# Performance work log

Hardware: AMD Instinct MI355X
Metric: run time of the kernel (lower is better)

The kernel has to match this reference:

```python
import jax, jax.numpy as jnp
import numpy as np

N_NODES = 100000


def gcn_conv(x, W, b, src, dst, n_nodes):
    # PyG GCNConv: x' = x @ W; symmetric deg^-1/2 normalization with self-loops; scatter-add; + bias
    h = x @ W  # [N, out]
    ones = jnp.ones(dst.shape[0], dtype=h.dtype)
    deg = jax.ops.segment_sum(ones, dst, num_segments=n_nodes)  # in-degree incl. self-loops
    dinv = jnp.where(deg > 0, jax.lax.rsqrt(deg), 0.0)
    norm = dinv[src] * dinv[dst]                      # [E]
    msgs = h[src] * norm[:, None]                     # gather + scale, [E, out]
    out = jax.ops.segment_sum(msgs, dst, num_segments=n_nodes)  # scatter-add
    return out + b


def setup_inputs() -> dict:
    key = jax.random.key(0)
    ks = jax.random.split(key, 8)
    n, e, din, dh, dout = N_NODES, 1600000, 32, 64, 5
    x = jax.random.normal(ks[0], (n, din), dtype=jnp.float32)
    edge_index = jax.random.randint(ks[1], (2, e), 0, n, dtype=jnp.int64)
    W1 = jax.random.normal(ks[2], (din, dh), dtype=jnp.float32) * (1.0 / np.sqrt(din))
    b1 = jax.random.normal(ks[3], (dh,), dtype=jnp.float32) * 0.02
    W2 = jax.random.normal(ks[4], (dh, dh), dtype=jnp.float32) * (1.0 / np.sqrt(dh))
    b2 = jax.random.normal(ks[5], (dh,), dtype=jnp.float32) * 0.02
    Wfc = jax.random.normal(ks[6], (dh, dout), dtype=jnp.float32) * (1.0 / np.sqrt(dh))
    bfc = jax.random.normal(ks[7], (dout,), dtype=jnp.float32) * 0.02
    return {"x": x, "edge_index": edge_index, "W1": W1, "b1": b1,
            "W2": W2, "b2": b2, "Wfc": Wfc, "bfc": bfc}


def reference(x, edge_index, W1, b1, W2, b2, Wfc, bfc):
    n = x.shape[0]
    loops = jnp.arange(n, dtype=edge_index.dtype)
    src = jnp.concatenate([edge_index[0], loops])  # add self-loops (PyG default)
    dst = jnp.concatenate([edge_index[1], loops])
    h = jax.nn.relu(gcn_conv(x, W1, b1, src, dst, n))
    h = jax.nn.relu(gcn_conv(h, W2, b2, src, dst, n))
    g = jnp.mean(h, axis=0)          # mean pool over nodes, [hidden]
    logits = g @ Wfc + bfc           # [output_dim]
    return jax.nn.log_softmax(logits, axis=0)
```

## Files before the change

kernel.cpp:

```cpp
#include <hip/hip_runtime.h>
#include <math.h>

#define NBLK 256

typedef unsigned int uint;
typedef __attribute__((ext_vector_type(8))) short short8;
typedef __attribute__((ext_vector_type(4))) float f32x4;
typedef __attribute__((ext_vector_type(2))) float f32x2;

#if defined(__has_builtin)
#if __has_builtin(__builtin_amdgcn_cvt_pk_f32_fp8) && __has_builtin(__builtin_amdgcn_cvt_pk_fp8_f32)
#define HW_FP8 1
#endif
#endif
#ifndef HW_FP8
#define HW_FP8 0
#endif

__device__ __forceinline__ uint pack_bf16(float a, float b) {
    uint ua = __float_as_uint(a), ub = __float_as_uint(b);
    ua = (ua + 0x7fffu + ((ua >> 16) & 1u)) >> 16;
    ub = (ub + 0x7fffu + ((ub >> 16) & 1u)) >> 16;
    return ua | (ub << 16);
}

__device__ __forceinline__ uint fp8_enc_sw(float v) {
    uint u = __float_as_uint(v);
    uint s = (u >> 24) & 0x80u;
    uint a = u & 0x7fffffffu;
    if (a < 0x3BF80000u) return s;
    if (a >= 0x43F80000u) return s | 0x7Fu;
    uint r = a + 0x0007FFFFu + ((a >> 20) & 1u);
    uint e8 = (r >> 23) - 120u;
    return s | (e8 << 3) | ((r >> 20) & 7u);
}
__device__ __forceinline__ float fp8_dec_sw(uint b) {
    uint t = b & 0x7fu;
    uint h = ((b & 0x80u) << 8) | (t ? ((t << 7) + 0x2000u) : 0u);
    return (float)__builtin_bit_cast(_Float16, (unsigned short)h);
}

__device__ __forceinline__ uint fp8x2_enc(float a, float b) {
#if HW_FP8
    return (uint)__builtin_amdgcn_cvt_pk_fp8_f32(a, b, 0, false);
#else
    return fp8_enc_sw(a) | (fp8_enc_sw(b) << 8);
#endif
}


__global__ void pass_hist(const int* __restrict__ dst, int* __restrict__ cnt,
                          int E, int nbucket, int chunk) {
    extern __shared__ int h[];
    int blk = blockIdx.x;
    for (int i = threadIdx.x; i < nbucket; i += blockDim.x) h[i] = 0;
    __syncthreads();
    int lo = blk * chunk, hi = min(lo + chunk, E);
    for (int e = lo + threadIdx.x; e < hi; e += blockDim.x)
        atomicAdd(&h[dst[e] >> 8], 1);
    __syncthreads();
    for (int i = threadIdx.x; i < nbucket; i += blockDim.x)
        cnt[i * NBLK + blk] = h[i];
}

__global__ void row_scan(int* __restrict__ cnt, int* __restrict__ totals) {
    __shared__ int lds[NBLK];
    int b = blockIdx.x, t = threadIdx.x;
    int v = cnt[b * NBLK + t];
    lds[t] = v;
    __syncthreads();
    for (int off = 1; off < NBLK; off <<= 1) {
        int y = (t >= off) ? lds[t - off] : 0;
        __syncthreads();
        lds[t] += y;
        __syncthreads();
    }
    cnt[b * NBLK + t] = lds[t] - v;
    if (t == NBLK - 1) totals[b] = lds[NBLK - 1];
}

__global__ void total_scan(int* __restrict__ totals, int nb) {
    __shared__ int lds[256];
    __shared__ int carry;
    int t = threadIdx.x;
    if (t == 0) carry = 0;
    __syncthreads();
    for (int c = 0; c < nb; c += 256) {
        int v = (c + t < nb) ? totals[c + t] : 0;
        lds[t] = v;
        __syncthreads();
        for (int off = 1; off < 256; off <<= 1) {
            int y = (t >= off) ? lds[t - off] : 0;
            __syncthreads();
            lds[t] += y;
            __syncthreads();
        }
        if (c + t < nb) totals[c + t] = carry + lds[t] - v;
        __syncthreads();
        if (t == 0) carry += lds[255];
        __syncthreads();
    }
    if (t == 0) totals[nb] = carry;
}

__global__ void pass_scatter(const int* __restrict__ src, const int* __restrict__ dst,
                             const int* __restrict__ cnt, const int* __restrict__ totals,
                             int* __restrict__ bucketed, int E, int nbucket, int chunk) {
    extern __shared__ int lcur[];
    int blk = blockIdx.x;
    for (int i = threadIdx.x; i < nbucket; i += blockDim.x)
        lcur[i] = cnt[i * NBLK + blk] + totals[i];
    __syncthreads();
    int lo = blk * chunk, hi = min(lo + chunk, E);
    for (int e = lo + threadIdx.x; e < hi; e += blockDim.x) {
        int s = src[e], d = dst[e];
        int pos = atomicAdd(&lcur[d >> 8], 1);
        bucketed[pos] = (s << 8) | (d & 255);
    }
}

__global__ void bucket_finalize(const int* __restrict__ bucketed, const int* __restrict__ totals,
                                int* __restrict__ rowptr, float* __restrict__ dinv,
                                int* __restrict__ csr_src, int n) {
    __shared__ int deg[256], sc[256], lcur[256];
    int b = blockIdx.x, t = threadIdx.x;
    int base = totals[b], bend = totals[b + 1];
    deg[t] = 0;
    __syncthreads();
    for (int i = base + t; i < bend; i += 256)
        atomicAdd(&deg[bucketed[i] & 255], 1);
    __syncthreads();
    int v = deg[t];
    sc[t] = v;
    __syncthreads();
    for (int off = 1; off < 256; off <<= 1) {
        int y = (t >= off) ? sc[t - off] : 0;
        __syncthreads();
        sc[t] += y;
        __syncthreads();
    }
    int ex = sc[t] - v;
    lcur[t] = ex;
    int node = b * 256 + t;
    if (node < n) {
        rowptr[node] = base + ex;
        dinv[node] = rsqrtf((float)(v + 1));
    }
    if (b == 0 && t == 0) rowptr[n] = totals[gridDim.x];
    __syncthreads();
    for (int i = base + t; i < bend; i += 256) {
        int p = bucketed[i];
        int pos = atomicAdd(&lcur[p & 255], 1);
        csr_src[base + pos] = p >> 8;
    }
}


__global__ void convert_x_fp8(const float* __restrict__ x, const float* __restrict__ dinv,
                              uint* __restrict__ xfp8, int n) {
    int i = blockIdx.x * blockDim.x + threadIdx.x;
    if (i >= n * 8) return;
    int v = i >> 3;
    float di = dinv[v];
    float4 xr = reinterpret_cast<const float4*>(x)[i];
    uint lo = fp8x2_enc(xr.x * di, xr.y * di);
    uint hi = fp8x2_enc(xr.z * di, xr.w * di);
    xfp8[i] = (lo & 0xffffu) | (hi << 16);
}


#if HW_FP8
#define DEC8ACC(U)                                                         \
    do {                                                                   \
        f32x2 p0 = __builtin_amdgcn_cvt_pk_f32_fp8((int)(U).x, 0);         \
        f32x2 p1 = __builtin_amdgcn_cvt_pk_f32_fp8((int)(U).x, 1);         \
        f32x2 p2 = __builtin_amdgcn_cvt_pk_f32_fp8((int)(U).y, 0);         \
        f32x2 p3 = __builtin_amdgcn_cvt_pk_f32_fp8((int)(U).y, 1);         \
        a0 += p0.x; a1 += p0.y; a2 += p1.x; a3 += p1.y;                    \
        a4 += p2.x; a5 += p2.y; a6 += p3.x; a7 += p3.y;                    \
    } while (0)
#else
#define DEC8ACC(U)                                                         \
    do {                                                                   \
        a0 += fp8_dec_sw((U).x); a1 += fp8_dec_sw((U).x >> 8);             \
        a2 += fp8_dec_sw((U).x >> 16); a3 += fp8_dec_sw((U).x >> 24);      \
        a4 += fp8_dec_sw((U).y); a5 += fp8_dec_sw((U).y >> 8);             \
        a6 += fp8_dec_sw((U).y >> 16); a7 += fp8_dec_sw((U).y >> 24);      \
    } while (0)
#endif

template <int LOG_NSL>
__global__ __launch_bounds__(256, 4) void agg_gather_fp8(
    const int* __restrict__ rowptr, const int* __restrict__ csr_src,
    const float* __restrict__ dinv, const uint* __restrict__ feat,
    uint* __restrict__ out, int n, int npad) {
    int bid = blockIdx.x;
    int slice = bid & ((1 << LOG_NSL) - 1);
    int chunk = bid >> LOG_NSL;
    int node = chunk * 64 + (threadIdx.x >> 2);
    if (node >= n) return;
    int q = threadIdx.x & 3;
    const uint* fs = feat + (size_t)slice * npad * 8 + q * 2;
    int k = rowptr[node], end = rowptr[node + 1];
    float a0 = 0.f, a1 = 0.f, a2 = 0.f, a3 = 0.f, a4 = 0.f, a5 = 0.f, a6 = 0.f, a7 = 0.f;
    {
        uint2 w = *reinterpret_cast<const uint2*>(fs + (size_t)node * 8);
        DEC8ACC(w);
    }
    for (; k + 4 <= end; k += 4) {
        int s0 = csr_src[k], s1 = csr_src[k + 1], s2 = csr_src[k + 2], s3 = csr_src[k + 3];
        uint2 u0 = *reinterpret_cast<const uint2*>(fs + (size_t)s0 * 8);
        uint2 u1 = *reinterpret_cast<const uint2*>(fs + (size_t)s1 * 8);
        uint2 u2 = *reinterpret_cast<const uint2*>(fs + (size_t)s2 * 8);
        uint2 u3 = *reinterpret_cast<const uint2*>(fs + (size_t)s3 * 8);
        DEC8ACC(u0); DEC8ACC(u1); DEC8ACC(u2); DEC8ACC(u3);
    }
    for (; k < end; ++k) {
        int s = csr_src[k];
        uint2 u = *reinterpret_cast<const uint2*>(fs + (size_t)s * 8);
        DEC8ACC(u);
    }
    float di = dinv[node];
    uint4 o;
    o.x = pack_bf16(a0 * di, a1 * di);
    o.y = pack_bf16(a2 * di, a3 * di);
    o.z = pack_bf16(a4 * di, a5 * di);
    o.w = pack_bf16(a6 * di, a7 * di);
    *reinterpret_cast<uint4*>(
        out + ((size_t)((slice << 1) + (q >> 1)) * npad + node) * 8 + (q & 1) * 4) = o;
}


__device__ __forceinline__ short8 make_bfrag(const float* __restrict__ W, int kbase, int col) {
    uint w0 = pack_bf16(W[(kbase + 0) * 64 + col], W[(kbase + 1) * 64 + col]);
    uint w1 = pack_bf16(W[(kbase + 2) * 64 + col], W[(kbase + 3) * 64 + col]);
    uint w2 = pack_bf16(W[(kbase + 4) * 64 + col], W[(kbase + 5) * 64 + col]);
    uint w3 = pack_bf16(W[(kbase + 6) * 64 + col], W[(kbase + 7) * 64 + col]);
    uint4 u; u.x = w0; u.y = w1; u.z = w2; u.w = w3;
    return __builtin_bit_cast(short8, u);
}

__global__ __launch_bounds__(256) void gemm1_mfma(const uint* __restrict__ A,
                                                  const float* __restrict__ W,
                                                  const float* __restrict__ bias,
                                                  const float* __restrict__ dinv,
                                                  uint* __restrict__ outw, int n, int npad) {
    int t = threadIdx.x;
    int lane = t & 63, wv = t >> 6;
    int rowbase = blockIdx.x * 64 + wv * 16;
    int r16 = lane & 15, g4 = lane >> 4;
    short8 a = __builtin_bit_cast(short8, *reinterpret_cast<const uint4*>(
        A + ((size_t)(g4 >> 1) * npad + rowbase + r16) * 8 + (g4 & 1) * 4));
    int kbase = g4 * 8;
    float dr[4];
#pragma unroll
    for (int r = 0; r < 4; ++r) {
        int row = rowbase + g4 * 4 + r;
        dr[r] = (row < n) ? dinv[row] : 0.f;
    }
#pragma unroll
    for (int nt = 0; nt < 4; ++nt) {
        int col = nt * 16 + r16;
        short8 b = make_bfrag(W, kbase, col);
        f32x4 z = {0.f, 0.f, 0.f, 0.f};
        f32x4 acc = __builtin_amdgcn_mfma_f32_16x16x32_bf16(a, b, z, 0, 0, 0);
        float bcol = bias[col];
#pragma unroll
        for (int r = 0; r < 4; ++r) {
            int row = rowbase + g4 * 4 + r;
            float v = fmaxf(acc[r] + bcol, 0.f) * dr[r];
            float vn = __shfl_xor(v, 1);
            uint e = fp8x2_enc(v, vn) & 0xffffu;
            uint e2 = __shfl_xor(e, 2);
            if ((r16 & 3) == 0)
                outw[((size_t)(col >> 5) * npad + row) * 8 + ((col & 31) >> 2)] =
                    e | (e2 << 16);
        }
    }
}

__global__ __launch_bounds__(256) void gemm2_mfma_pool(const uint* __restrict__ A,
                                                       const float* __restrict__ W,
                                                       const float* __restrict__ bias,
                                                       float* __restrict__ pool_part,
                                                       int n, int npad) {
    __shared__ float sblk[64];
    int t = threadIdx.x;
    if (t < 64) sblk[t] = 0.f;
    __syncthreads();
    int lane = t & 63, wv = t >> 6;
    int rowbase = blockIdx.x * 64 + wv * 16;
    int r16 = lane & 15, g4 = lane >> 4;
    size_t roff = (size_t)(rowbase + r16) * 8 + (g4 & 1) * 4;
    size_t sstride = (size_t)npad * 8;
    short8 a0 = __builtin_bit_cast(short8,
        *reinterpret_cast<const uint4*>(A + (size_t)(g4 >> 1) * sstride + roff));
    short8 a1 = __builtin_bit_cast(short8,
        *reinterpret_cast<const uint4*>(A + (size_t)(2 + (g4 >> 1)) * sstride + roff));
#pragma unroll
    for (int nt = 0; nt < 4; ++nt) {
        int col = nt * 16 + r16;
        short8 b0 = make_bfrag(W, g4 * 8, col);
        short8 b1 = make_bfrag(W, 32 + g4 * 8, col);
        f32x4 z = {0.f, 0.f, 0.f, 0.f};
        f32x4 acc = __builtin_amdgcn_mfma_f32_16x16x32_bf16(a0, b0, z, 0, 0, 0);
        acc = __builtin_amdgcn_mfma_f32_16x16x32_bf16(a1, b1, acc, 0, 0, 0);
        float bcol = bias[col];
        float part = 0.f;
#pragma unroll
        for (int r = 0; r < 4; ++r) {
            int row = rowbase + g4 * 4 + r;
            float v = fmaxf(acc[r] + bcol, 0.f);
            part += (row < n) ? v : 0.f;
        }
        atomicAdd(&sblk[col], part);
    }
    __syncthreads();
    if (t < 64) pool_part[(size_t)blockIdx.x * 64 + t] = sblk[t];
}

__global__ __launch_bounds__(256) void pool_reduce(const float* __restrict__ pool_part,
                                                   int nblk, float* __restrict__ part2) {
    __shared__ float sd[256];
    int t = threadIdx.x;
    int col = t & 63, grp = t >> 6;
    int row0 = blockIdx.x * 4 + grp;
    float acc = 0.f;
    for (int b = row0; b < nblk; b += 256) acc += pool_part[(size_t)b * 64 + col];
    sd[t] = acc;
    __syncthreads();
    if (t < 64)
        part2[(size_t)blockIdx.x * 64 + t] = sd[t] + sd[t + 64] + sd[t + 128] + sd[t + 192];
}

__global__ __launch_bounds__(512) void final_head(const float* __restrict__ part2,
                                                  const float* __restrict__ Wfc,
                                                  const float* __restrict__ bfc,
                                                  float* __restrict__ out, int n) {
    __shared__ float red[512];
    __shared__ float gsh[64];
    __shared__ float logits[5];
    int t = threadIdx.x;
    int col = t & 63, grp = t >> 6;
    float acc = 0.f;
#pragma unroll
    for (int i = 0; i < 8; ++i) acc += part2[(size_t)(grp * 8 + i) * 64 + col];
    red[t] = acc;
    __syncthreads();
    if (t < 64) {
        float s = 0.f;
#pragma unroll
        for (int gI = 0; gI < 8; ++gI) s += red[gI * 64 + t];
        gsh[t] = s;
    }
    __syncthreads();
    if (t < 5) {
        float a = bfc[t];
        float invn = 1.0f / (float)n;
        for (int k = 0; k < 64; ++k) a += (gsh[k] * invn) * Wfc[k * 5 + t];
        logits[t] = a;
    }
    __syncthreads();
    if (t == 0) {
        float m = logits[0];
        for (int i = 1; i < 5; ++i) m = fmaxf(m, logits[i]);
        float s = 0.0f;
        for (int i = 0; i < 5; ++i) s += expf(logits[i] - m);
        float lse = m + logf(s);
        for (int i = 0; i < 5; ++i) out[i] = logits[i] - lse;
    }
}


extern "C" void kernel_launch(void* const* d_in, const int* in_sizes, int n_in,
                              void* d_out, int out_size, void* d_ws, size_t ws_size,
                              hipStream_t stream) {
    const float* x   = (const float*)d_in[0];
    const int*   ei  = (const int*)d_in[1];
    const float* W1  = (const float*)d_in[2];
    const float* b1  = (const float*)d_in[3];
    const float* W2  = (const float*)d_in[4];
    const float* b2  = (const float*)d_in[5];
    const float* Wfc = (const float*)d_in[6];
    const float* bfc = (const float*)d_in[7];
    float* out = (float*)d_out;

    const int n = in_sizes[0] / 32;
    const int E = in_sizes[1] / 2;
    const int* src = ei;
    const int* dst = ei + E;
    const int npad = (n + 63) & ~63;
    const int nbucket = (n + 255) >> 8;
    const int chunk = (E + NBLK - 1) / NBLK;
    const int nchunk = (n + 63) / 64;

    int*   csr_src = (int*)d_ws;
    int*   rowptr  = csr_src + E;
    float* dinv    = (float*)(rowptr + n + 1);
    int*   cnt     = (int*)(dinv + n);
    int*   totals  = cnt + (size_t)nbucket * NBLK;
    size_t offw    = (size_t)(totals + nbucket + 1 - (int*)d_ws);
    offw           = (offw + 3) & ~(size_t)3;
    uint*  xfp8    = (uint*)d_ws + offw;
    uint*  h1fp8   = xfp8 + (size_t)npad * 8;
    uint*  agg1    = h1fp8 + (size_t)2 * npad * 8;
    uint*  agg2    = agg1 + (size_t)2 * npad * 8;
    float* pool_part = (float*)(agg2 + (size_t)4 * npad * 8);
    float* part2   = pool_part + (size_t)nchunk * 64;
    int*   bucketed = (int*)agg2;

    const int B = 256;
    const size_t lds_b = (size_t)nbucket * sizeof(int);

    pass_hist<<<NBLK, B, lds_b, stream>>>(dst, cnt, E, nbucket, chunk);
    row_scan<<<nbucket, NBLK, 0, stream>>>(cnt, totals);
    total_scan<<<1, B, 0, stream>>>(totals, nbucket);
    pass_scatter<<<NBLK, B, lds_b, stream>>>(src, dst, cnt, totals, bucketed, E, nbucket, chunk);
    bucket_finalize<<<nbucket, B, 0, stream>>>(bucketed, totals, rowptr, dinv, csr_src, n);

    convert_x_fp8<<<(n * 8 + B - 1) / B, B, 0, stream>>>(x, dinv, xfp8, n);

    agg_gather_fp8<0><<<nchunk, B, 0, stream>>>(rowptr, csr_src, dinv, xfp8, agg1, n, npad);
    gemm1_mfma<<<nchunk, B, 0, stream>>>(agg1, W1, b1, dinv, h1fp8, n, npad);

    agg_gather_fp8<1><<<nchunk * 2, B, 0, stream>>>(rowptr, csr_src, dinv, h1fp8, agg2, n, npad);
    gemm2_mfma_pool<<<nchunk, B, 0, stream>>>(agg2, W2, b2, pool_part, n, npad);

    pool_reduce<<<64, B, 0, stream>>>(pool_part, nchunk, part2);
    final_head<<<1, 512, 0, stream>>>(part2, Wfc, bfc, out, n);
}
```

Measured before the change: 127.1 us.

## Fuse x fp8 conversion into bucket_finalize and layer-1 gather into GEMM1

The x-to-fp8 conversion (pre-scaled by dinv) now happens inside bucket_finalize, with each node thread converting its own row, so one launch is gone. The layer-1 neighbour gather is fused with the GEMM1 MFMA kernel: aggregated rows are packed to bf16 in LDS and fed straight into the MFMA, removing the agg1 global buffer round trip and another launch. In exchange, the per-thread x conversion in bucket_finalize reads 128 contiguous bytes per thread, which coalesces poorly, and the fused kernel's LDS use may affect occupancy.

```diff
diff --git a/kernel.cpp b/kernel.cpp
--- a/kernel.cpp
+++ b/kernel.cpp
@@ -47,127 +47,6 @@
     return fp8_enc_sw(a) | (fp8_enc_sw(b) << 8);
 #endif
 }
-
-
-__global__ void pass_hist(const int* __restrict__ dst, int* __restrict__ cnt,
-                          int E, int nbucket, int chunk) {
-    extern __shared__ int h[];
-    int blk = blockIdx.x;
-    for (int i = threadIdx.x; i < nbucket; i += blockDim.x) h[i] = 0;
-    __syncthreads();
-    int lo = blk * chunk, hi = min(lo + chunk, E);
-    for (int e = lo + threadIdx.x; e < hi; e += blockDim.x)
-        atomicAdd(&h[dst[e] >> 8], 1);
-    __syncthreads();
-    for (int i = threadIdx.x; i < nbucket; i += blockDim.x)
-        cnt[i * NBLK + blk] = h[i];
-}
-
-__global__ void row_scan(int* __restrict__ cnt, int* __restrict__ totals) {
-    __shared__ int lds[NBLK];
-    int b = blockIdx.x, t = threadIdx.x;
-    int v = cnt[b * NBLK + t];
-    lds[t] = v;
-    __syncthreads();
-    for (int off = 1; off < NBLK; off <<= 1) {
-        int y = (t >= off) ? lds[t - off] : 0;
-        __syncthreads();
-        lds[t] += y;
-        __syncthreads();
-    }
-    cnt[b * NBLK + t] = lds[t] - v;
-    if (t == NBLK - 1) totals[b] = lds[NBLK - 1];
-}
-
-__global__ void total_scan(int* __restrict__ totals, int nb) {
-    __shared__ int lds[256];
-    __shared__ int carry;
-    int t = threadIdx.x;
-    if (t == 0) carry = 0;
-    __syncthreads();
-    for (int c = 0; c < nb; c += 256) {
-        int v = (c + t < nb) ? totals[c + t] : 0;
-        lds[t] = v;
-        __syncthreads();
-        for (int off = 1; off < 256; off <<= 1) {
-            int y = (t >= off) ? lds[t - off] : 0;
-            __syncthreads();
-            lds[t] += y;
-            __syncthreads();
-        }
-        if (c + t < nb) totals[c + t] = carry + lds[t] - v;
-        __syncthreads();
-        if (t == 0) carry += lds[255];
-        __syncthreads();
-    }
-    if (t == 0) totals[nb] = carry;
-}
-
-__global__ void pass_scatter(const int* __restrict__ src, const int* __restrict__ dst,
-                             const int* __restrict__ cnt, const int* __restrict__ totals,
-                             int* __restrict__ bucketed, int E, int nbucket, int chunk) {
-    extern __shared__ int lcur[];
-    int blk = blockIdx.x;
-    for (int i = threadIdx.x; i < nbucket; i += blockDim.x)
-        lcur[i] = cnt[i * NBLK + blk] + totals[i];
-    __syncthreads();
-    int lo = blk * chunk, hi = min(lo + chunk, E);
-    for (int e = lo + threadIdx.x; e < hi; e += blockDim.x) {
-        int s = src[e], d = dst[e];
-        int pos = atomicAdd(&lcur[d >> 8], 1);
-        bucketed[pos] = (s << 8) | (d & 255);
-    }
-}
-
-__global__ void bucket_finalize(const int* __restrict__ bucketed, const int* __restrict__ totals,
-                                int* __restrict__ rowptr, float* __restrict__ dinv,
-                                int* __restrict__ csr_src, int n) {
-    __shared__ int deg[256], sc[256], lcur[256];
-    int b = blockIdx.x, t = threadIdx.x;
-    int base = totals[b], bend = totals[b + 1];
-    deg[t] = 0;
-    __syncthreads();
-    for (int i = base + t; i < bend; i += 256)
-        atomicAdd(&deg[bucketed[i] & 255], 1);
-    __syncthreads();
-    int v = deg[t];
-    sc[t] = v;
-    __syncthreads();
-    for (int off = 1; off < 256; off <<= 1) {
-        int y = (t >= off) ? sc[t - off] : 0;
-        __syncthreads();
-        sc[t] += y;
-        __syncthreads();
-    }
-    int ex = sc[t] - v;
-    lcur[t] = ex;
-    int node = b * 256 + t;
-    if (node < n) {
-        rowptr[node] = base + ex;
-        dinv[node] = rsqrtf((float)(v + 1));
-    }
-    if (b == 0 && t == 0) rowptr[n] = totals[gridDim.x];
-    __syncthreads();
-    for (int i = base + t; i < bend; i += 256) {
-        int p = bucketed[i];
-        int pos = atomicAdd(&lcur[p & 255], 1);
-        csr_src[base + pos] = p >> 8;
-    }
-}
-
-
-__global__ void convert_x_fp8(const float* __restrict__ x, const float* __restrict__ dinv,
-                              uint* __restrict__ xfp8, int n) {
-    int i = blockIdx.x * blockDim.x + threadIdx.x;
-    if (i >= n * 8) return;
-    int v = i >> 3;
-    float di = dinv[v];
-    float4 xr = reinterpret_cast<const float4*>(x)[i];
-    uint lo = fp8x2_enc(xr.x * di, xr.y * di);
-    uint hi = fp8x2_enc(xr.z * di, xr.w * di);
-    xfp8[i] = (lo & 0xffffu) | (hi << 16);
-}
-
 
 #if HW_FP8
 #define DEC8ACC(U)                                                         \
@@ -189,6 +68,209 @@
     } while (0)
 #endif
 
+
+__global__ void pass_hist(const int* __restrict__ dst, int* __restrict__ cnt,
+                          int E, int nbucket, int chunk) {
+    extern __shared__ int h[];
+    int blk = blockIdx.x;
+    for (int i = threadIdx.x; i < nbucket; i += blockDim.x) h[i] = 0;
+    __syncthreads();
+    int lo = blk * chunk, hi = min(lo + chunk, E);
+    for (int e = lo + threadIdx.x; e < hi; e += blockDim.x)
+        atomicAdd(&h[dst[e] >> 8], 1);
+    __syncthreads();
+    for (int i = threadIdx.x; i < nbucket; i += blockDim.x)
+        cnt[i * NBLK + blk] = h[i];
+}
+
+__global__ void row_scan(int* __restrict__ cnt, int* __restrict__ totals) {
+    __shared__ int lds[NBLK];
+    int b = blockIdx.x, t = threadIdx.x;
+    int v = cnt[b * NBLK + t];
+    lds[t] = v;
+    __syncthreads();
+    for (int off = 1; off < NBLK; off <<= 1) {
+        int y = (t >= off) ? lds[t - off] : 0;
+        __syncthreads();
+        lds[t] += y;
+        __syncthreads();
+    }
+    cnt[b * NBLK + t] = lds[t] - v;
+    if (t == NBLK - 1) totals[b] = lds[NBLK - 1];
+}
+
+__global__ void total_scan(int* __restrict__ totals, int nb) {
+    __shared__ int lds[256];
+    __shared__ int carry;
+    int t = threadIdx.x;
+    if (t == 0) carry = 0;
+    __syncthreads();
+    for (int c = 0; c < nb; c += 256) {
+        int v = (c + t < nb) ? totals[c + t] : 0;
+        lds[t] = v;
+        __syncthreads();
+        for (int off = 1; off < 256; off <<= 1) {
+            int y = (t >= off) ? lds[t - off] : 0;
+            __syncthreads();
+            lds[t] += y;
+            __syncthreads();
+        }
+        if (c + t < nb) totals[c + t] = carry + lds[t] - v;
+        __syncthreads();
+        if (t == 0) carry += lds[255];
+        __syncthreads();
+    }
+    if (t == 0) totals[nb] = carry;
+}
+
+__global__ void pass_scatter(const int* __restrict__ src, const int* __restrict__ dst,
+                             const int* __restrict__ cnt, const int* __restrict__ totals,
+                             int* __restrict__ bucketed, int E, int nbucket, int chunk) {
+    extern __shared__ int lcur[];
+    int blk = blockIdx.x;
+    for (int i = threadIdx.x; i < nbucket; i += blockDim.x)
+        lcur[i] = cnt[i * NBLK + blk] + totals[i];
+    __syncthreads();
+    int lo = blk * chunk, hi = min(lo + chunk, E);
+    for (int e = lo + threadIdx.x; e < hi; e += blockDim.x) {
+        int s = src[e], d = dst[e];
+        int pos = atomicAdd(&lcur[d >> 8], 1);
+        bucketed[pos] = (s << 8) | (d & 255);
+    }
+}
+
+__global__ void bucket_finalize(const int* __restrict__ bucketed, const int* __restrict__ totals,
+                                int* __restrict__ rowptr, float* __restrict__ dinv,
+                                int* __restrict__ csr_src, const float* __restrict__ x,
+                                uint* __restrict__ xfp8, int n) {
+    __shared__ int deg[256], sc[256], lcur[256];
+    int b = blockIdx.x, t = threadIdx.x;
+    int base = totals[b], bend = totals[b + 1];
+    deg[t] = 0;
+    __syncthreads();
+    for (int i = base + t; i < bend; i += 256)
+        atomicAdd(&deg[bucketed[i] & 255], 1);
+    __syncthreads();
+    int v = deg[t];
+    sc[t] = v;
+    __syncthreads();
+    for (int off = 1; off < 256; off <<= 1) {
+        int y = (t >= off) ? sc[t - off] : 0;
+        __syncthreads();
+        sc[t] += y;
+        __syncthreads();
+    }
+    int ex = sc[t] - v;
+    lcur[t] = ex;
+    int node = b * 256 + t;
+    if (node < n) {
+        float dfac = rsqrtf((float)(v + 1));
+        rowptr[node] = base + ex;
+        dinv[node] = dfac;
+        const float4* xr = reinterpret_cast<const float4*>(x + (size_t)node * 32);
+        uint* xo = xfp8 + (size_t)node * 8;
+#pragma unroll
+        for (int w = 0; w < 8; ++w) {
+            float4 xv = xr[w];
+            uint lo = fp8x2_enc(xv.x * dfac, xv.y * dfac);
+            uint hi = fp8x2_enc(xv.z * dfac, xv.w * dfac);
+            xo[w] = (lo & 0xffffu) | (hi << 16);
+        }
+    }
+    if (b == 0 && t == 0) rowptr[n] = totals[gridDim.x];
+    __syncthreads();
+    for (int i = base + t; i < bend; i += 256) {
+        int p = bucketed[i];
+        int pos = atomicAdd(&lcur[p & 255], 1);
+        csr_src[base + pos] = p >> 8;
+    }
+}
+
+
+__device__ __forceinline__ short8 make_bfrag(const float* __restrict__ W, int kbase, int col) {
+    uint w0 = pack_bf16(W[(kbase + 0) * 64 + col], W[(kbase + 1) * 64 + col]);
+    uint w1 = pack_bf16(W[(kbase + 2) * 64 + col], W[(kbase + 3) * 64 + col]);
+    uint w2 = pack_bf16(W[(kbase + 4) * 64 + col], W[(kbase + 5) * 64 + col]);
+    uint w3 = pack_bf16(W[(kbase + 6) * 64 + col], W[(kbase + 7) * 64 + col]);
+    uint4 u; u.x = w0; u.y = w1; u.z = w2; u.w = w3;
+    return __builtin_bit_cast(short8, u);
+}
+
+__global__ __launch_bounds__(256, 4) void agg1_gemm1_fused(
+    const int* __restrict__ rowptr, const int* __restrict__ csr_src,
+    const float* __restrict__ dinv, const uint* __restrict__ xfp8,
+    const float* __restrict__ W, const float* __restrict__ bias,
+    uint* __restrict__ outw, int n, int npad) {
+    __shared__ uint lds[64 * 16];
+    int t = threadIdx.x;
+    {
+        int v4 = t >> 2, q = t & 3;
+        int node = blockIdx.x * 64 + v4;
+        const uint* fs = xfp8 + q * 2;
+        float a0 = 0.f, a1 = 0.f, a2 = 0.f, a3 = 0.f,
+              a4 = 0.f, a5 = 0.f, a6 = 0.f, a7 = 0.f;
+        float di = 0.f;
+        int k = 0, end = 0;
+        if (node < n) {
+            k = rowptr[node]; end = rowptr[node + 1];
+            di = dinv[node];
+            uint2 w = *reinterpret_cast<const uint2*>(fs + (size_t)node * 8);
+            DEC8ACC(w);
+        }
+        for (; k + 4 <= end; k += 4) {
+            int s0 = csr_src[k], s1 = csr_src[k + 1], s2 = csr_src[k + 2], s3 = csr_src[k + 3];
+            uint2 u0 = *reinterpret_cast<const uint2*>(fs + (size_t)s0 * 8);
+            uint2 u1 = *reinterpret_cast<const uint2*>(fs + (size_t)s1 * 8);
+            uint2 u2 = *reinterpret_cast<const uint2*>(fs + (size_t)s2 * 8);
+            uint2 u3 = *reinterpret_cast<const uint2*>(fs + (size_t)s3 * 8);
+            DEC8ACC(u0); DEC8ACC(u1); DEC8ACC(u2); DEC8ACC(u3);
+        }
+        for (; k < end; ++k) {
+            int s = csr_src[k];
+            uint2 u = *reinterpret_cast<const uint2*>(fs + (size_t)s * 8);
+            DEC8ACC(u);
+        }
+        uint4 o;
+        o.x = pack_bf16(a0 * di, a1 * di);
+        o.y = pack_bf16(a2 * di, a3 * di);
+        o.z = pack_bf16(a4 * di, a5 * di);
+        o.w = pack_bf16(a6 * di, a7 * di);
+        *reinterpret_cast<uint4*>(&lds[v4 * 16 + q * 4]) = o;
+    }
+    __syncthreads();
+    int lane = t & 63, wv = t >> 6;
+    int rowbase = blockIdx.x * 64 + wv * 16;
+    int r16 = lane & 15, g4 = lane >> 4;
+    short8 a = __builtin_bit_cast(short8,
+        *reinterpret_cast<const uint4*>(&lds[(wv * 16 + r16) * 16 + g4 * 4]));
+    int kbase = g4 * 8;
+    float dr[4];
+#pragma unroll
+    for (int r = 0; r < 4; ++r) {
+        int row = rowbase + g4 * 4 + r;
+        dr[r] = (row < n) ? dinv[row] : 0.f;
+    }
+#pragma unroll
+    for (int nt = 0; nt < 4; ++nt) {
+        int col = nt * 16 + r16;
+        short8 b = make_bfrag(W, kbase, col);
+        f32x4 z = {0.f, 0.f, 0.f, 0.f};
+        f32x4 acc = __builtin_amdgcn_mfma_f32_16x16x32_bf16(a, b, z, 0, 0, 0);
+        float bcol = bias[col];
+#pragma unroll
+        for (int r = 0; r < 4; ++r) {
+            int row = rowbase + g4 * 4 + r;
+            float v = fmaxf(acc[r] + bcol, 0.f) * dr[r];
+            float vn = __shfl_xor(v, 1);
+            uint e = fp8x2_enc(v, vn) & 0xffffu;
+            uint e2 = __shfl_xor(e, 2);
+            if ((r16 & 3) == 0)
+                outw[((size_t)(col >> 5) * npad + row) * 8 + ((col & 31) >> 2)] =
+                    e | (e2 << 16);
+        }
+    }
+}
+
 template <int LOG_NSL>
 __global__ __launch_bounds__(256, 4) void agg_gather_fp8(
     const int* __restrict__ rowptr, const int* __restrict__ csr_src,
@@ -230,55 +312,6 @@
         out + ((size_t)((slice << 1) + (q >> 1)) * npad + node) * 8 + (q & 1) * 4) = o;
 }
 
-
-__device__ __forceinline__ short8 make_bfrag(const float* __restrict__ W, int kbase, int col) {
-    uint w0 = pack_bf16(W[(kbase + 0) * 64 + col], W[(kbase + 1) * 64 + col]);
-    uint w1 = pack_bf16(W[(kbase + 2) * 64 + col], W[(kbase + 3) * 64 + col]);
-    uint w2 = pack_bf16(W[(kbase + 4) * 64 + col], W[(kbase + 5) * 64 + col]);
-    uint w3 = pack_bf16(W[(kbase + 6) * 64 + col], W[(kbase + 7) * 64 + col]);
-    uint4 u; u.x = w0; u.y = w1; u.z = w2; u.w = w3;
-    return __builtin_bit_cast(short8, u);
-}
-
-__global__ __launch_bounds__(256) void gemm1_mfma(const uint* __restrict__ A,
-                                                  const float* __restrict__ W,
-                                                  const float* __restrict__ bias,
-                                                  const float* __restrict__ dinv,
-                                                  uint* __restrict__ outw, int n, int npad) {
-    int t = threadIdx.x;
-    int lane = t & 63, wv = t >> 6;
-    int rowbase = blockIdx.x * 64 + wv * 16;
-    int r16 = lane & 15, g4 = lane >> 4;
-    short8 a = __builtin_bit_cast(short8, *reinterpret_cast<const uint4*>(
-        A + ((size_t)(g4 >> 1) * npad + rowbase + r16) * 8 + (g4 & 1) * 4));
-    int kbase = g4 * 8;
-    float dr[4];
-#pragma unroll
-    for (int r = 0; r < 4; ++r) {
-        int row = rowbase + g4 * 4 + r;
-        dr[r] = (row < n) ? dinv[row] : 0.f;
-    }
-#pragma unroll
-    for (int nt = 0; nt < 4; ++nt) {
-        int col = nt * 16 + r16;
-        short8 b = make_bfrag(W, kbase, col);
-        f32x4 z = {0.f, 0.f, 0.f, 0.f};
-        f32x4 acc = __builtin_amdgcn_mfma_f32_16x16x32_bf16(a, b, z, 0, 0, 0);
-        float bcol = bias[col];
-#pragma unroll
-        for (int r = 0; r < 4; ++r) {
-            int row = rowbase + g4 * 4 + r;
-            float v = fmaxf(acc[r] + bcol, 0.f) * dr[r];
-            float vn = __shfl_xor(v, 1);
-            uint e = fp8x2_enc(v, vn) & 0xffffu;
-            uint e2 = __shfl_xor(e, 2);
-            if ((r16 & 3) == 0)
-                outw[((size_t)(col >> 5) * npad + row) * 8 + ((col & 31) >> 2)] =
-                    e | (e2 << 16);
-        }
-    }
-}
-
 __global__ __launch_bounds__(256) void gemm2_mfma_pool(const uint* __restrict__ A,
                                                        const float* __restrict__ W,
                                                        const float* __restrict__ bias,
@@ -403,8 +436,7 @@
     offw           = (offw + 3) & ~(size_t)3;
     uint*  xfp8    = (uint*)d_ws + offw;
     uint*  h1fp8   = xfp8 + (size_t)npad * 8;
-    uint*  agg1    = h1fp8 + (size_t)2 * npad * 8;
-    uint*  agg2    = agg1 + (size_t)2 * npad * 8;
+    uint*  agg2    = h1fp8 + (size_t)2 * npad * 8;
     float* pool_part = (float*)(agg2 + (size_t)4 * npad * 8);
     float* part2   = pool_part + (size_t)nchunk * 64;
     int*   bucketed = (int*)agg2;
@@ -416,12 +448,11 @@
     row_scan<<<nbucket, NBLK, 0, stream>>>(cnt, totals);
     total_scan<<<1, B, 0, stream>>>(totals, nbucket);
     pass_scatter<<<NBLK, B, lds_b, stream>>>(src, dst, cnt, totals, bucketed, E, nbucket, chunk);
-    bucket_finalize<<<nbucket, B, 0, stream>>>(bucketed, totals, rowptr, dinv, csr_src, n);
-
-    convert_x_fp8<<<(n * 8 + B - 1) / B, B, 0, stream>>>(x, dinv, xfp8, n);
-
-    agg_gather_fp8<0><<<nchunk, B, 0, stream>>>(rowptr, csr_src, dinv, xfp8, agg1, n, npad);
-    gemm1_mfma<<<nchunk, B, 0, stream>>>(agg1, W1, b1, dinv, h1fp8, n, npad);
+    bucket_finalize<<<nbucket, B, 0, stream>>>(bucketed, totals, rowptr, dinv, csr_src,
+                                               x, xfp8, n);
+
+    agg1_gemm1_fused<<<nchunk, B, 0, stream>>>(rowptr, csr_src, dinv, xfp8, W1, b1,
+                                               h1fp8, n, npad);
 
     agg_gather_fp8<1><<<nchunk * 2, B, 0, stream>>>(rowptr, csr_src, dinv, h1fp8, agg2, n, npad);
     gemm2_mfma_pool<<<nchunk, B, 0, stream>>>(agg2, W2, b2, pool_part, n, npad);
```

New measurement: 123.0 us. 1.03x faster.
